# Optimization experiments

Hardware: AMD Instinct MI355X
Metric: run time of the kernel (lower is better)

## Reference

```python
import jax, jax.numpy as jnp
import numpy as np

B, N, D = 64, 2048, 128  # batch, neighbors, embedding_dim (= region_dim)


def setup_inputs() -> dict:
    key = jax.random.key(0)
    ks = jax.random.split(key, 8)
    inv_sqrt_d = 1.0 / np.sqrt(D).astype(np.float32)
    return {
        "e_i": jax.random.normal(ks[0], (B, D), jnp.float32),
        "e_j": jax.random.normal(ks[1], (B, N, D), jnp.float32),
        "imp_j": jax.random.uniform(ks[2], (B, N), jnp.float32),
        "R_lk": jax.random.normal(ks[3], (D, D), jnp.float32),
        "W_q": jax.random.normal(ks[4], (D, D), jnp.float32) * inv_sqrt_d,
        "W_k": jax.random.normal(ks[5], (D, D), jnp.float32) * inv_sqrt_d,
        "W_v": jax.random.normal(ks[6], (D, D), jnp.float32) * inv_sqrt_d,
        "omega": jax.random.normal(ks[7], (D,), jnp.float32),
    }


def reference(e_i, e_j, imp_j, R_lk, W_q, W_k, W_v, omega):
    # torch nn.Linear(x) = x @ W.T; weights are [out, in] = [D, D]
    q = e_i @ W_q.T                                   # [B, D]
    k = jnp.einsum('bnd,ed->bne', e_j, W_k)           # [B, N, D]
    # additive tanh attention score sigma_ij = tanh(q_i + k_j) . omega
    sigma = jnp.tanh(q[:, None, :] + k) @ omega       # [B, N]
    exp_s = jnp.exp(sigma)
    denom = jnp.sum(exp_s, axis=1, keepdims=True) + 1e-9
    a = imp_j * exp_s / denom                         # [B, N]  (a_ij, squeezed)
    v = jnp.einsum('bnd,ed->bne', e_j, W_v)           # [B, N, D]
    # A_i_t = sum_n a_ij * v_j  (identical math to A_i_l in the source)
    A_l = jnp.einsum('bn,bnd->bd', a, v)              # [B, D]
    # sum_n R[l,k] * a[b,n] * v[b,n,k] = R[l,k] * A_l[b,k]  -- fused, no [B,N,D,D]
    A_lk = R_lk[None, :, :] * A_l[:, None, :]         # [B, D, D]
    return A_l, A_lk, A_l
```

## Files before the change

kernel.cpp:

```cpp
#include <hip/hip_runtime.h>
#include <stdint.h>

#define BB 64
#define NN 2048
#define DD 128
#define ROWS 64
#define PADB 136

typedef __attribute__((ext_vector_type(8))) short short8;
typedef __attribute__((ext_vector_type(4))) float f32x4;

__device__ __forceinline__ unsigned short f2bf_rtne(float x) {
    union { float f; unsigned int u; } v; v.f = x;
    unsigned int r = v.u + 0x7fffu + ((v.u >> 16) & 1u);
    return (unsigned short)(r >> 16);
}
__device__ __forceinline__ float bf2f(unsigned short h) {
    union { unsigned int u; float f; } v; v.u = ((unsigned int)h) << 16;
    return v.f;
}
__device__ __forceinline__ float tanh_fast(float x) {
    float ax = fabsf(x);
    float e  = __expf(-2.f * ax);
    float t  = (1.f - e) / (1.f + e);
    return copysignf(t, x);
}

__global__ __launch_bounds__(128) void aegis_prep(
    const float* __restrict__ e_i, const float* __restrict__ Wq,
    float* __restrict__ qbuf)
{
    __shared__ float eis[DD];
    const int t = threadIdx.x, b = blockIdx.x;
    eis[t] = e_i[b * DD + t];
    __syncthreads();
    float acc = 0.f;
    const float4* wr = reinterpret_cast<const float4*>(Wq + t * DD);
    const float4* ev = reinterpret_cast<const float4*>(eis);
    #pragma unroll 8
    for (int i = 0; i < 32; ++i) {
        float4 w = wr[i], e = ev[i];
        acc = fmaf(w.x, e.x, acc); acc = fmaf(w.y, e.y, acc);
        acc = fmaf(w.z, e.z, acc); acc = fmaf(w.w, e.w, acc);
    }
    qbuf[b * DD + t] = acc;
}

__global__ __launch_bounds__(256) void aegis_main(
    const float* __restrict__ e_j, const float* __restrict__ imp,
    const float* __restrict__ Wk,  const float* __restrict__ omega,
    const float* __restrict__ qbuf,
    float* __restrict__ sprime, float* __restrict__ denom)
{
    __shared__ unsigned short Ehi[ROWS][PADB];
    __shared__ unsigned short Elo[ROWS][PADB];
    __shared__ float sig[ROWS][4];
    __shared__ float wrow[ROWS];
    __shared__ float scol[DD];

    const int t     = threadIdx.x;
    const int blk   = blockIdx.x;
    const int b     = blk >> 5;
    const int chunk = blk & 31;
    const int row0  = chunk * ROWS;

    const int lane = t & 63;
    const int w    = t >> 6;
    const int lr   = lane & 15;
    const int lg   = lane >> 4;

    short8 Bhi[2][4], Blo[2][4];
    #pragma unroll
    for (int ct = 0; ct < 2; ++ct) {
        const int e = 32 * w + 16 * ct + lr;
        const float* wr = Wk + e * DD + lg * 8;
        #pragma unroll
        for (int ks = 0; ks < 4; ++ks) {
            float4 x0 = *reinterpret_cast<const float4*>(wr + ks * 32);
            float4 x1 = *reinterpret_cast<const float4*>(wr + ks * 32 + 4);
            float xs[8] = {x0.x, x0.y, x0.z, x0.w, x1.x, x1.y, x1.z, x1.w};
            short8 h, l;
            #pragma unroll
            for (int j = 0; j < 8; ++j) {
                unsigned short hb = f2bf_rtne(xs[j]);
                float rem = xs[j] - bf2f(hb);
                h[j] = (short)hb;
                l[j] = (short)f2bf_rtne(rem);
            }
            Bhi[ct][ks] = h; Blo[ct][ks] = l;
        }
    }

    {
        const float4* src = reinterpret_cast<const float4*>(
            e_j + ((size_t)(b * NN + row0)) * DD);
        #pragma unroll
        for (int i = 0; i < 8; ++i) {
            int idx = t + i * 256;
            int rr  = idx >> 5;
            int cc  = (idx & 31) * 4;
            float4 v = src[idx];
            float xs[4] = {v.x, v.y, v.z, v.w};
            unsigned short hs[4], ls[4];
            #pragma unroll
            for (int j = 0; j < 4; ++j) {
                hs[j] = f2bf_rtne(xs[j]);
                ls[j] = f2bf_rtne(xs[j] - bf2f(hs[j]));
            }
            uint2 ph, pl;
            ph.x = (unsigned)hs[0] | ((unsigned)hs[1] << 16);
            ph.y = (unsigned)hs[2] | ((unsigned)hs[3] << 16);
            pl.x = (unsigned)ls[0] | ((unsigned)ls[1] << 16);
            pl.y = (unsigned)ls[2] | ((unsigned)ls[3] << 16);
            *reinterpret_cast<uint2*>(&Ehi[rr][cc]) = ph;
            *reinterpret_cast<uint2*>(&Elo[rr][cc]) = pl;
        }
    }

    float qv[2], ov[2];
    #pragma unroll
    for (int ct = 0; ct < 2; ++ct) {
        int c = 32 * w + 16 * ct + lr;
        qv[ct] = qbuf[b * DD + c];
        ov[ct] = omega[c];
    }
    __syncthreads();

    #pragma unroll 1
    for (int rt = 0; rt < 4; ++rt) {
        f32x4 acc0 = {0.f, 0.f, 0.f, 0.f};
        f32x4 acc1 = {0.f, 0.f, 0.f, 0.f};
        #pragma unroll
        for (int ks = 0; ks < 4; ++ks) {
            const int arow = rt * 16 + lr;
            short8 ah = *reinterpret_cast<const short8*>(&Ehi[arow][ks * 32 + lg * 8]);
            short8 al = *reinterpret_cast<const short8*>(&Elo[arow][ks * 32 + lg * 8]);
            acc0 = __builtin_amdgcn_mfma_f32_16x16x32_bf16(ah, Bhi[0][ks], acc0, 0, 0, 0);
            acc1 = __builtin_amdgcn_mfma_f32_16x16x32_bf16(ah, Bhi[1][ks], acc1, 0, 0, 0);
            acc0 = __builtin_amdgcn_mfma_f32_16x16x32_bf16(ah, Blo[0][ks], acc0, 0, 0, 0);
            acc1 = __builtin_amdgcn_mfma_f32_16x16x32_bf16(ah, Blo[1][ks], acc1, 0, 0, 0);
            acc0 = __builtin_amdgcn_mfma_f32_16x16x32_bf16(al, Bhi[0][ks], acc0, 0, 0, 0);
            acc1 = __builtin_amdgcn_mfma_f32_16x16x32_bf16(al, Bhi[1][ks], acc1, 0, 0, 0);
        }
        float sp[4];
        #pragma unroll
        for (int i = 0; i < 4; ++i) {
            float x0 = qv[0] + acc0[i];
            float x1 = qv[1] + acc1[i];
            sp[i] = fmaf(ov[0], tanh_fast(x0), ov[1] * tanh_fast(x1));
        }
        #pragma unroll
        for (int m = 1; m < 16; m <<= 1) {
            #pragma unroll
            for (int i = 0; i < 4; ++i) sp[i] += __shfl_xor(sp[i], m);
        }
        if (lr == 0) {
            #pragma unroll
            for (int i = 0; i < 4; ++i) sig[rt * 16 + 4 * lg + i][w] = sp[i];
        }
    }
    __syncthreads();

    if (t < ROWS) {
        float sg = sig[t][0] + sig[t][1] + sig[t][2] + sig[t][3];
        float es = __expf(sg);
        wrow[t]  = es * imp[b * NN + row0 + t];
        float d = es;
        #pragma unroll
        for (int m = 1; m < 64; m <<= 1) d += __shfl_xor(d, m);
        if (t == 0) atomicAdd(&denom[b], d);
    }
    __syncthreads();

    {
        int d  = t & 127;
        int hf = t >> 7;
        float part = 0.f;
        #pragma unroll
        for (int rr = hf * 32; rr < hf * 32 + 32; ++rr) {
            float ev = bf2f(Ehi[rr][d]) + bf2f(Elo[rr][d]);
            part = fmaf(wrow[rr], ev, part);
        }
        if (hf == 0) scol[d] = part;
        __syncthreads();
        if (hf == 1) atomicAdd(&sprime[b * DD + d], part + scol[d]);
    }
}

__global__ __launch_bounds__(128) void aegis_epi1(
    const float* __restrict__ sprime, const float* __restrict__ denomv,
    const float* __restrict__ Wv, float* __restrict__ out)
{
    __shared__ float sn[DD];
    const int t = threadIdx.x, b = blockIdx.x;
    sn[t] = sprime[b * DD + t] / (denomv[b] + 1e-9f);
    __syncthreads();
    float acc = 0.f;
    const float4* wr = reinterpret_cast<const float4*>(Wv + t * DD);
    const float4* sv = reinterpret_cast<const float4*>(sn);
    #pragma unroll 8
    for (int i = 0; i < 32; ++i) {
        float4 w = wr[i], e = sv[i];
        acc = fmaf(w.x, e.x, acc); acc = fmaf(w.y, e.y, acc);
        acc = fmaf(w.z, e.z, acc); acc = fmaf(w.w, e.w, acc);
    }
    out[b * DD + t] = acc;
    out[8192 + 1048576 + b * DD + t] = acc;
}

__global__ __launch_bounds__(256) void aegis_epi2(
    const float* __restrict__ R, const float* __restrict__ out0,
    float* __restrict__ outk)
{
    const int b  = blockIdx.x >> 2;
    const int sl = blockIdx.x & 3;
    const int t  = threadIdx.x;
    const float* al = out0 + b * DD;
    float4* dst = reinterpret_cast<float4*>(outk + (size_t)b * DD * DD + sl * 4096);
    const float4* rsrc = reinterpret_cast<const float4*>(R + sl * 4096);
    #pragma unroll
    for (int i = 0; i < 4; ++i) {
        int idx = t + i * 256;
        float4 r = rsrc[idx];
        int k0 = (idx & 31) * 4;
        float4 o;
        o.x = r.x * al[k0];     o.y = r.y * al[k0 + 1];
        o.z = r.z * al[k0 + 2]; o.w = r.w * al[k0 + 3];
        dst[idx] = o;
    }
}

extern "C" void kernel_launch(void* const* d_in, const int* in_sizes, int n_in,
                              void* d_out, int out_size, void* d_ws, size_t ws_size,
                              hipStream_t stream) {
    const float* e_i = (const float*)d_in[0];
    const float* e_j = (const float*)d_in[1];
    const float* imp = (const float*)d_in[2];
    const float* R   = (const float*)d_in[3];
    const float* Wq  = (const float*)d_in[4];
    const float* Wk  = (const float*)d_in[5];
    const float* Wv  = (const float*)d_in[6];
    const float* om  = (const float*)d_in[7];

    float* out    = (float*)d_out;
    float* sprime = (float*)d_ws;
    float* denom  = (float*)((char*)d_ws + 32768);
    float* qbuf   = out + 8192;

    hipMemsetAsync(d_ws, 0, 32768 + 256, stream);
    aegis_prep<<<dim3(BB), dim3(128), 0, stream>>>(e_i, Wq, qbuf);
    aegis_main<<<dim3(BB * 32), dim3(256), 0, stream>>>(
        e_j, imp, Wk, om, qbuf, sprime, denom);
    aegis_epi1<<<dim3(BB), dim3(128), 0, stream>>>(sprime, denom, Wv, out);
    aegis_epi2<<<dim3(BB * 4), dim3(256), 0, stream>>>(R, out, out + 8192);
}
```

Baseline: 156.1 us.

## Precompute split-bf16 Wk once, swizzle LDS, merge epilogues, drop memset

Wk is converted to hi/lo bf16 fragments once in the prep kernel and stored in the output scratch region, so each main block loads ready fragments instead of reconverting them. The main kernel now processes two 64-row chunks per block, which halves the grid and the number of atomics. It also replaces padded LDS rows with an XOR swizzle. Zeroing of the accumulators moves into the prep kernel, which removes the memset launch, and the two epilogue kernels are merged into one. The risks are more serial work per block, fewer blocks in flight, and reliance on the scratch area in out being overwritten later.

New measurement: 159.4 us. 1.02x slower.

```diff
diff --git a/kernel.cpp b/kernel.cpp
--- a/kernel.cpp
+++ b/kernel.cpp
@@ -5,7 +5,7 @@
 #define NN 2048
 #define DD 128
 #define ROWS 64
-#define PADB 136
+#define CPB 2
 
 typedef __attribute__((ext_vector_type(8))) short short8;
 typedef __attribute__((ext_vector_type(4))) float f32x4;
@@ -26,203 +26,241 @@
     return copysignf(t, x);
 }
 
-__global__ __launch_bounds__(128) void aegis_prep(
+__global__ __launch_bounds__(256) void aegis_prep(
     const float* __restrict__ e_i, const float* __restrict__ Wq,
-    float* __restrict__ qbuf)
+    const float* __restrict__ Wk,
+    float* __restrict__ qbuf, unsigned short* __restrict__ Bhig,
+    unsigned short* __restrict__ Blog,
+    float* __restrict__ sprime, float* __restrict__ denom)
 {
     __shared__ float eis[DD];
-    const int t = threadIdx.x, b = blockIdx.x;
-    eis[t] = e_i[b * DD + t];
-    __syncthreads();
-    float acc = 0.f;
-    const float4* wr = reinterpret_cast<const float4*>(Wq + t * DD);
-    const float4* ev = reinterpret_cast<const float4*>(eis);
-    #pragma unroll 8
-    for (int i = 0; i < 32; ++i) {
-        float4 w = wr[i], e = ev[i];
-        acc = fmaf(w.x, e.x, acc); acc = fmaf(w.y, e.y, acc);
-        acc = fmaf(w.z, e.z, acc); acc = fmaf(w.w, e.w, acc);
-    }
-    qbuf[b * DD + t] = acc;
-}
-
-__global__ __launch_bounds__(256) void aegis_main(
+    const int t = threadIdx.x, blk = blockIdx.x;
+    if (blk < 8) {
+        const int tid = blk * 256 + t;
+        const int lr = tid & 15, lg = (tid >> 4) & 3, ks = (tid >> 6) & 3, et = tid >> 8;
+        const int e = et * 16 + lr, k = ks * 32 + lg * 8;
+        const float* src = Wk + e * DD + k;
+        float4 x0 = *reinterpret_cast<const float4*>(src);
+        float4 x1 = *reinterpret_cast<const float4*>(src + 4);
+        float xs[8] = {x0.x, x0.y, x0.z, x0.w, x1.x, x1.y, x1.z, x1.w};
+        short8 h, l;
+        #pragma unroll
+        for (int j = 0; j < 8; ++j) {
+            unsigned short hb = f2bf_rtne(xs[j]);
+            float rem = xs[j] - bf2f(hb);
+            h[j] = (short)hb;
+            l[j] = (short)f2bf_rtne(rem);
+        }
+        *reinterpret_cast<short8*>(Bhig + (size_t)tid * 8) = h;
+        *reinterpret_cast<short8*>(Blog + (size_t)tid * 8) = l;
+    } else {
+        const int b = blk - 8;
+        if (t < DD) eis[t] = e_i[b * DD + t];
+        __syncthreads();
+        if (t < DD) {
+            float acc = 0.f;
+            const float4* wr = reinterpret_cast<const float4*>(Wq + t * DD);
+            const float4* ev = reinterpret_cast<const float4*>(eis);
+            #pragma unroll 8
+            for (int i = 0; i < 32; ++i) {
+                float4 w = wr[i], e = ev[i];
+                acc = fmaf(w.x, e.x, acc); acc = fmaf(w.y, e.y, acc);
+                acc = fmaf(w.z, e.z, acc); acc = fmaf(w.w, e.w, acc);
+            }
+            qbuf[b * DD + t] = acc;
+            sprime[b * DD + t] = 0.f;
+        }
+        if (t == 0) denom[b] = 0.f;
+    }
+}
+
+__global__ __launch_bounds__(256, 4) void aegis_main(
     const float* __restrict__ e_j, const float* __restrict__ imp,
-    const float* __restrict__ Wk,  const float* __restrict__ omega,
-    const float* __restrict__ qbuf,
+    const float* __restrict__ omega, const float* __restrict__ qbuf,
+    const unsigned short* __restrict__ Bhig, const unsigned short* __restrict__ Blog,
     float* __restrict__ sprime, float* __restrict__ denom)
 {
-    __shared__ unsigned short Ehi[ROWS][PADB];
-    __shared__ unsigned short Elo[ROWS][PADB];
+    __shared__ unsigned short Ehi[ROWS * DD];
+    __shared__ unsigned short Elo[ROWS * DD];
     __shared__ float sig[ROWS][4];
     __shared__ float wrow[ROWS];
     __shared__ float scol[DD];
 
-    const int t     = threadIdx.x;
-    const int blk   = blockIdx.x;
-    const int b     = blk >> 5;
-    const int chunk = blk & 31;
-    const int row0  = chunk * ROWS;
-
+    const int t    = threadIdx.x;
+    const int b    = blockIdx.x >> 4;
+    const int cb   = blockIdx.x & 15;
     const int lane = t & 63;
     const int w    = t >> 6;
     const int lr   = lane & 15;
     const int lg   = lane >> 4;
 
-    short8 Bhi[2][4], Blo[2][4];
+    short8 Bh[2][4], Bl[2][4];
     #pragma unroll
-    for (int ct = 0; ct < 2; ++ct) {
-        const int e = 32 * w + 16 * ct + lr;
-        const float* wr = Wk + e * DD + lg * 8;
+    for (int ct = 0; ct < 2; ++ct)
         #pragma unroll
         for (int ks = 0; ks < 4; ++ks) {
-            float4 x0 = *reinterpret_cast<const float4*>(wr + ks * 32);
-            float4 x1 = *reinterpret_cast<const float4*>(wr + ks * 32 + 4);
-            float xs[8] = {x0.x, x0.y, x0.z, x0.w, x1.x, x1.y, x1.z, x1.w};
-            short8 h, l;
-            #pragma unroll
-            for (int j = 0; j < 8; ++j) {
-                unsigned short hb = f2bf_rtne(xs[j]);
-                float rem = xs[j] - bf2f(hb);
-                h[j] = (short)hb;
-                l[j] = (short)f2bf_rtne(rem);
-            }
-            Bhi[ct][ks] = h; Blo[ct][ks] = l;
-        }
-    }
-
-    {
-        const float4* src = reinterpret_cast<const float4*>(
-            e_j + ((size_t)(b * NN + row0)) * DD);
-        #pragma unroll
-        for (int i = 0; i < 8; ++i) {
-            int idx = t + i * 256;
-            int rr  = idx >> 5;
-            int cc  = (idx & 31) * 4;
-            float4 v = src[idx];
-            float xs[4] = {v.x, v.y, v.z, v.w};
-            unsigned short hs[4], ls[4];
-            #pragma unroll
-            for (int j = 0; j < 4; ++j) {
-                hs[j] = f2bf_rtne(xs[j]);
-                ls[j] = f2bf_rtne(xs[j] - bf2f(hs[j]));
-            }
-            uint2 ph, pl;
-            ph.x = (unsigned)hs[0] | ((unsigned)hs[1] << 16);
-            ph.y = (unsigned)hs[2] | ((unsigned)hs[3] << 16);
-            pl.x = (unsigned)ls[0] | ((unsigned)ls[1] << 16);
-            pl.y = (unsigned)ls[2] | ((unsigned)ls[3] << 16);
-            *reinterpret_cast<uint2*>(&Ehi[rr][cc]) = ph;
-            *reinterpret_cast<uint2*>(&Elo[rr][cc]) = pl;
-        }
-    }
+            const int fi = (((2 * w + ct) * 4 + ks) * 4 + lg) * 16 + lr;
+            Bh[ct][ks] = *reinterpret_cast<const short8*>(Bhig + (size_t)fi * 8);
+            Bl[ct][ks] = *reinterpret_cast<const short8*>(Blog + (size_t)fi * 8);
+        }
 
     float qv[2], ov[2];
     #pragma unroll
     for (int ct = 0; ct < 2; ++ct) {
-        int c = 32 * w + 16 * ct + lr;
+        const int c = 32 * w + 16 * ct + lr;
         qv[ct] = qbuf[b * DD + c];
         ov[ct] = omega[c];
     }
-    __syncthreads();
+
+    const int d  = t & 127;
+    const int hf = t >> 7;
+    float sacc = 0.f, den_local = 0.f;
 
     #pragma unroll 1
-    for (int rt = 0; rt < 4; ++rt) {
-        f32x4 acc0 = {0.f, 0.f, 0.f, 0.f};
-        f32x4 acc1 = {0.f, 0.f, 0.f, 0.f};
-        #pragma unroll
-        for (int ks = 0; ks < 4; ++ks) {
+    for (int c = 0; c < CPB; ++c) {
+        const int row0 = (cb * CPB + c) * ROWS;
+        __syncthreads();
+
+        {
+            const float4* src = reinterpret_cast<const float4*>(
+                e_j + ((size_t)(b * NN + row0)) * DD);
+            #pragma unroll
+            for (int i = 0; i < 8; ++i) {
+                const int idx = t + i * 256;
+                const int rr  = idx >> 5;
+                const int bc  = (idx & 31) * 8;
+                float4 v = src[idx];
+                float xs[4] = {v.x, v.y, v.z, v.w};
+                unsigned short hs[4], ls[4];
+                #pragma unroll
+                for (int j = 0; j < 4; ++j) {
+                    hs[j] = f2bf_rtne(xs[j]);
+                    ls[j] = f2bf_rtne(xs[j] - bf2f(hs[j]));
+                }
+                uint2 ph, pl;
+                ph.x = (unsigned)hs[0] | ((unsigned)hs[1] << 16);
+                ph.y = (unsigned)hs[2] | ((unsigned)hs[3] << 16);
+                pl.x = (unsigned)ls[0] | ((unsigned)ls[1] << 16);
+                pl.y = (unsigned)ls[2] | ((unsigned)ls[3] << 16);
+                const int off = rr * 256 + (bc ^ ((rr & 7) << 4));
+                *reinterpret_cast<uint2*>(reinterpret_cast<char*>(Ehi) + off) = ph;
+                *reinterpret_cast<uint2*>(reinterpret_cast<char*>(Elo) + off) = pl;
+            }
+        }
+        __syncthreads();
+
+        #pragma unroll 1
+        for (int rt = 0; rt < 4; ++rt) {
+            f32x4 a0 = {0.f, 0.f, 0.f, 0.f};
+            f32x4 a1 = {0.f, 0.f, 0.f, 0.f};
             const int arow = rt * 16 + lr;
-            short8 ah = *reinterpret_cast<const short8*>(&Ehi[arow][ks * 32 + lg * 8]);
-            short8 al = *reinterpret_cast<const short8*>(&Elo[arow][ks * 32 + lg * 8]);
-            acc0 = __builtin_amdgcn_mfma_f32_16x16x32_bf16(ah, Bhi[0][ks], acc0, 0, 0, 0);
-            acc1 = __builtin_amdgcn_mfma_f32_16x16x32_bf16(ah, Bhi[1][ks], acc1, 0, 0, 0);
-            acc0 = __builtin_amdgcn_mfma_f32_16x16x32_bf16(ah, Blo[0][ks], acc0, 0, 0, 0);
-            acc1 = __builtin_amdgcn_mfma_f32_16x16x32_bf16(ah, Blo[1][ks], acc1, 0, 0, 0);
-            acc0 = __builtin_amdgcn_mfma_f32_16x16x32_bf16(al, Bhi[0][ks], acc0, 0, 0, 0);
-            acc1 = __builtin_amdgcn_mfma_f32_16x16x32_bf16(al, Bhi[1][ks], acc1, 0, 0, 0);
-        }
-        float sp[4];
-        #pragma unroll
-        for (int i = 0; i < 4; ++i) {
-            float x0 = qv[0] + acc0[i];
-            float x1 = qv[1] + acc1[i];
-            sp[i] = fmaf(ov[0], tanh_fast(x0), ov[1] * tanh_fast(x1));
-        }
-        #pragma unroll
-        for (int m = 1; m < 16; m <<= 1) {
-            #pragma unroll
-            for (int i = 0; i < 4; ++i) sp[i] += __shfl_xor(sp[i], m);
-        }
-        if (lr == 0) {
-            #pragma unroll
-            for (int i = 0; i < 4; ++i) sig[rt * 16 + 4 * lg + i][w] = sp[i];
-        }
-    }
-    __syncthreads();
-
-    if (t < ROWS) {
-        float sg = sig[t][0] + sig[t][1] + sig[t][2] + sig[t][3];
-        float es = __expf(sg);
-        wrow[t]  = es * imp[b * NN + row0 + t];
-        float d = es;
-        #pragma unroll
-        for (int m = 1; m < 64; m <<= 1) d += __shfl_xor(d, m);
-        if (t == 0) atomicAdd(&denom[b], d);
-    }
-    __syncthreads();
-
-    {
-        int d  = t & 127;
-        int hf = t >> 7;
-        float part = 0.f;
-        #pragma unroll
-        for (int rr = hf * 32; rr < hf * 32 + 32; ++rr) {
-            float ev = bf2f(Ehi[rr][d]) + bf2f(Elo[rr][d]);
-            part = fmaf(wrow[rr], ev, part);
-        }
-        if (hf == 0) scol[d] = part;
-        __syncthreads();
-        if (hf == 1) atomicAdd(&sprime[b * DD + d], part + scol[d]);
-    }
-}
-
-__global__ __launch_bounds__(128) void aegis_epi1(
+            const int rbase = arow * 256;
+            const int rsw   = (lr & 7) << 4;
+            #pragma unroll
+            for (int ks = 0; ks < 4; ++ks) {
+                const int off = rbase + ((ks * 64 + lg * 16) ^ rsw);
+                short8 ah = *reinterpret_cast<const short8*>(
+                    reinterpret_cast<const char*>(Ehi) + off);
+                short8 al = *reinterpret_cast<const short8*>(
+                    reinterpret_cast<const char*>(Elo) + off);
+                a0 = __builtin_amdgcn_mfma_f32_16x16x32_bf16(ah, Bh[0][ks], a0, 0, 0, 0);
+                a1 = __builtin_amdgcn_mfma_f32_16x16x32_bf16(ah, Bh[1][ks], a1, 0, 0, 0);
+                a0 = __builtin_amdgcn_mfma_f32_16x16x32_bf16(ah, Bl[0][ks], a0, 0, 0, 0);
+                a1 = __builtin_amdgcn_mfma_f32_16x16x32_bf16(ah, Bl[1][ks], a1, 0, 0, 0);
+                a0 = __builtin_amdgcn_mfma_f32_16x16x32_bf16(al, Bh[0][ks], a0, 0, 0, 0);
+                a1 = __builtin_amdgcn_mfma_f32_16x16x32_bf16(al, Bh[1][ks], a1, 0, 0, 0);
+            }
+            float sp[4];
+            #pragma unroll
+            for (int i = 0; i < 4; ++i) {
+                float x0 = qv[0] + a0[i];
+                float x1 = qv[1] + a1[i];
+                sp[i] = fmaf(ov[0], tanh_fast(x0), ov[1] * tanh_fast(x1));
+            }
+            #pragma unroll
+            for (int m = 1; m < 16; m <<= 1) {
+                #pragma unroll
+                for (int i = 0; i < 4; ++i) sp[i] += __shfl_xor(sp[i], m);
+            }
+            if (lr == 0) {
+                #pragma unroll
+                for (int i = 0; i < 4; ++i) sig[rt * 16 + 4 * lg + i][w] = sp[i];
+            }
+        }
+        __syncthreads();
+
+        if (t < ROWS) {
+            float sg = sig[t][0] + sig[t][1] + sig[t][2] + sig[t][3];
+            float es = __expf(sg);
+            wrow[t]  = es * imp[b * NN + row0 + t];
+            float ds = es;
+            #pragma unroll
+            for (int m = 1; m < 64; m <<= 1) ds += __shfl_xor(ds, m);
+            if (t == 0) den_local += ds;
+        }
+        __syncthreads();
+
+        {
+            float part = 0.f;
+            #pragma unroll
+            for (int rr = hf * 32; rr < hf * 32 + 32; ++rr) {
+                const int off = rr * 256 + ((2 * d) ^ ((rr & 7) << 4));
+                float ev = bf2f(*reinterpret_cast<const unsigned short*>(
+                               reinterpret_cast<const char*>(Ehi) + off))
+                         + bf2f(*reinterpret_cast<const unsigned short*>(
+                               reinterpret_cast<const char*>(Elo) + off));
+                part = fmaf(wrow[rr], ev, part);
+            }
+            sacc += part;
+        }
+    }
+
+    if (hf == 0) scol[d] = sacc;
+    __syncthreads();
+    if (hf == 1) atomicAdd(&sprime[b * DD + d], sacc + scol[d]);
+    if (t == 0) atomicAdd(&denom[b], den_local);
+}
+
+__global__ __launch_bounds__(256) void aegis_epi(
     const float* __restrict__ sprime, const float* __restrict__ denomv,
-    const float* __restrict__ Wv, float* __restrict__ out)
+    const float* __restrict__ Wv, const float* __restrict__ R,
+    float* __restrict__ out)
 {
     __shared__ float sn[DD];
+    __shared__ float alred[DD][2];
+    __shared__ float al[DD];
     const int t = threadIdx.x, b = blockIdx.x;
-    sn[t] = sprime[b * DD + t] / (denomv[b] + 1e-9f);
-    __syncthreads();
-    float acc = 0.f;
-    const float4* wr = reinterpret_cast<const float4*>(Wv + t * DD);
-    const float4* sv = reinterpret_cast<const float4*>(sn);
-    #pragma unroll 8
-    for (int i = 0; i < 32; ++i) {
-        float4 w = wr[i], e = sv[i];
-        acc = fmaf(w.x, e.x, acc); acc = fmaf(w.y, e.y, acc);
-        acc = fmaf(w.z, e.z, acc); acc = fmaf(w.w, e.w, acc);
-    }
-    out[b * DD + t] = acc;
-    out[8192 + 1048576 + b * DD + t] = acc;
-}
-
-__global__ __launch_bounds__(256) void aegis_epi2(
-    const float* __restrict__ R, const float* __restrict__ out0,
-    float* __restrict__ outk)
-{
-    const int b  = blockIdx.x >> 2;
-    const int sl = blockIdx.x & 3;
-    const int t  = threadIdx.x;
-    const float* al = out0 + b * DD;
-    float4* dst = reinterpret_cast<float4*>(outk + (size_t)b * DD * DD + sl * 4096);
-    const float4* rsrc = reinterpret_cast<const float4*>(R + sl * 4096);
+
+    if (t < DD) sn[t] = sprime[b * DD + t] / (denomv[b] + 1e-9f);
+    __syncthreads();
+    {
+        const int l = t >> 1, h = t & 1;
+        const float4* wr = reinterpret_cast<const float4*>(Wv + l * DD + h * 64);
+        const float4* sv = reinterpret_cast<const float4*>(sn + h * 64);
+        float acc = 0.f;
+        #pragma unroll 8
+        for (int i = 0; i < 16; ++i) {
+            float4 w = wr[i], e = sv[i];
+            acc = fmaf(w.x, e.x, acc); acc = fmaf(w.y, e.y, acc);
+            acc = fmaf(w.z, e.z, acc); acc = fmaf(w.w, e.w, acc);
+        }
+        alred[l][h] = acc;
+    }
+    __syncthreads();
+    if (t < DD) {
+        float v = alred[t][0] + alred[t][1];
+        al[t] = v;
+        out[b * DD + t] = v;
+        out[8192 + 1048576 + b * DD + t] = v;
+    }
+    __syncthreads();
+    float4* dst = reinterpret_cast<float4*>(out + 8192 + (size_t)b * DD * DD);
+    const float4* rsrc = reinterpret_cast<const float4*>(R);
     #pragma unroll
-    for (int i = 0; i < 4; ++i) {
-        int idx = t + i * 256;
+    for (int i = 0; i < 16; ++i) {
+        const int idx = t + i * 256;
         float4 r = rsrc[idx];
-        int k0 = (idx & 31) * 4;
+        const int k0 = (idx & 31) * 4;
         float4 o;
         o.x = r.x * al[k0];     o.y = r.y * al[k0 + 1];
         o.z = r.z * al[k0 + 2]; o.w = r.w * al[k0 + 3];
@@ -245,12 +283,14 @@
     float* out    = (float*)d_out;
     float* sprime = (float*)d_ws;
     float* denom  = (float*)((char*)d_ws + 32768);
-    float* qbuf   = out + 8192;
-
-    hipMemsetAsync(d_ws, 0, 32768 + 256, stream);
-    aegis_prep<<<dim3(BB), dim3(128), 0, stream>>>(e_i, Wq, qbuf);
-    aegis_main<<<dim3(BB * 32), dim3(256), 0, stream>>>(
-        e_j, imp, Wk, om, qbuf, sprime, denom);
-    aegis_epi1<<<dim3(BB), dim3(128), 0, stream>>>(sprime, denom, Wv, out);
-    aegis_epi2<<<dim3(BB * 4), dim3(256), 0, stream>>>(R, out, out + 8192);
-}
+
+    float* qbuf = out + 8192;
+    unsigned short* Bhig = (unsigned short*)(out + 8192 + 8192);
+    unsigned short* Blog = Bhig + 16384;
+
+    aegis_prep<<<dim3(72), dim3(256), 0, stream>>>(
+        e_i, Wq, Wk, qbuf, Bhig, Blog, sprime, denom);
+    aegis_main<<<dim3(BB * 16), dim3(256), 0, stream>>>(
+        e_j, imp, om, qbuf, Bhig, Blog, sprime, denom);
+    aegis_epi<<<dim3(BB), dim3(256), 0, stream>>>(sprime, denom, Wv, R, out);
+}
```
